# Kernel optimization log

Hardware: AMD Instinct MI355X
Metric: run time of the kernel (lower is better)

## Reference

```python
import jax, jax.numpy as jnp
import numpy as np

L2_REG = 0.01  # config['l2_reg']


def setup_inputs() -> dict:
    key = jax.random.key(0)
    k1, k2, k3, k4 = jax.random.split(key, 4)
    N = 16384
    risk_pred = jax.random.normal(k1, (N, 1), dtype=jnp.float32)
    y = jax.random.uniform(k2, (N, 1), dtype=jnp.float32)  # survival times
    e = jax.random.randint(k3, (N, 1), 0, 2, dtype=jnp.int32)  # event indicator
    W = jax.random.normal(k4, (512, 256), dtype=jnp.float32)  # model weight for L2 reg
    return {"risk_pred": risk_pred, "y": y, "e": e, "W": W}


def reference(risk_pred, y, e, W):
    # mask[i, j] = 1 if y[j] <= y[i] else 0  (torch: mask[y.T - y > 0] = 0)
    mask = (y.T - y <= 0).astype(risk_pred.dtype)  # (N, N)
    exp_r = jnp.exp(risk_pred)                      # (N, 1), broadcasts over rows
    num = jnp.sum(exp_r * mask, axis=0)             # (N,) risk-set weighted sum per column
    den = jnp.sum(mask, axis=0)                     # (N,) risk-set size per column
    log_loss = jnp.log(num / den).reshape(-1, 1)    # (N, 1)
    ef = e.astype(risk_pred.dtype)
    neg_log_loss = -jnp.sum((risk_pred - log_loss) * ef) / jnp.sum(ef)
    l2_loss = L2_REG * jnp.linalg.norm(W)           # Regularization(order=2)
    return neg_log_loss + l2_loss
```

## Files before the change

kernel.cpp:

```cpp
#include <hip/hip_runtime.h>

#define L2_REG 0.01f
#define NBIN 1024
#define MAXB 64


__global__ __launch_bounds__(256) void cox_hist(const float* __restrict__ rp,
                                                const float* __restrict__ y,
                                                const float* __restrict__ W,
                                                int* __restrict__ cnt,
                                                float* __restrict__ sum,
                                                float* __restrict__ by,
                                                float* __restrict__ be,
                                                float* __restrict__ wpart) {
    const int b = blockIdx.x;
    if (b < 64) {
        const int i = b * 256 + threadIdx.x;
        const float yi = y[i];
        const float ei = __expf(rp[i]);
        int bin = (int)(yi * (float)NBIN);
        bin = min(max(bin, 0), NBIN - 1);
        atomicAdd(&sum[bin], ei);
        const int pos = atomicAdd(&cnt[bin], 1);
        if (pos < MAXB) {
            by[bin * MAXB + pos] = yi;
            be[bin * MAXB + pos] = ei;
        }
    } else {
        __shared__ float l[4];
        const float4* W4 = reinterpret_cast<const float4*>(W) + (b - 64) * 512;
        float s = 0.f;
#pragma unroll
        for (int k = 0; k < 2; ++k) {
            float4 w = W4[k * 256 + threadIdx.x];
            s = fmaf(w.x, w.x, s); s = fmaf(w.y, w.y, s);
            s = fmaf(w.z, w.z, s); s = fmaf(w.w, w.w, s);
        }
#pragma unroll
        for (int off = 32; off; off >>= 1) s += __shfl_down(s, off, 64);
        const int lane = threadIdx.x & 63, wave = threadIdx.x >> 6;
        if (lane == 0) l[wave] = s;
        __syncthreads();
        if (threadIdx.x == 0) wpart[b - 64] = l[0] + l[1] + l[2] + l[3];
    }
}

__global__ __launch_bounds__(1024) void cox_scan(const int* __restrict__ cnt,
                                                 const float* __restrict__ sum,
                                                 const float* __restrict__ wpart,
                                                 float* __restrict__ sufc,
                                                 float* __restrict__ sufs,
                                                 float* __restrict__ acc,
                                                 int* __restrict__ cnt2) {
    __shared__ float sc[NBIN];
    __shared__ float sm[NBIN];
    const int t = threadIdx.x;
    sc[t] = (float)cnt[t];
    sm[t] = sum[t];
    __syncthreads();
#pragma unroll
    for (int s = 1; s < NBIN; s <<= 1) {
        const float a = (t + s < NBIN) ? sc[t + s] : 0.f;
        const float c = (t + s < NBIN) ? sm[t + s] : 0.f;
        __syncthreads();
        sc[t] += a; sm[t] += c;
        __syncthreads();
    }
    sufc[t] = sc[t];
    sufs[t] = sm[t];
    if (t == 0) {
        sufc[NBIN] = 0.f; sufs[NBIN] = 0.f;
        acc[0] = 0.f; acc[1] = 0.f; cnt2[0] = 0;
    }
    if (t < 64) {
        float wv = wpart[t];
#pragma unroll
        for (int off = 32; off; off >>= 1) wv += __shfl_down(wv, off, 64);
        if (t == 0) acc[2] = wv;
    }
}

__global__ __launch_bounds__(64) void cox_terms(const float* __restrict__ rp,
                                                const float* __restrict__ y,
                                                const int* __restrict__ e,
                                                const int* __restrict__ cnt,
                                                const float* __restrict__ by,
                                                const float* __restrict__ be,
                                                const float* __restrict__ sufc,
                                                const float* __restrict__ sufs,
                                                float* __restrict__ acc,
                                                int* __restrict__ cnt2,
                                                float* __restrict__ out) {
    const int j = blockIdx.x * 64 + threadIdx.x;
    const float yj = y[j];
    int bin = (int)(yj * (float)NBIN);
    bin = min(max(bin, 0), NBIN - 1);
    float den = sufc[bin + 1];
    float num = sufs[bin + 1];
    const int nb = min(cnt[bin], MAXB);
    const float4* by4 = reinterpret_cast<const float4*>(by + bin * MAXB);
    const float4* be4 = reinterpret_cast<const float4*>(be + bin * MAXB);
    for (int p = 0; p < nb; p += 4) {
        const float4 yv = by4[p >> 2];
        const float4 ev = be4[p >> 2];
        const float m0 = (yv.x >= yj) ? 1.f : 0.f;
        const float m1 = ((p + 1 < nb) && (yv.y >= yj)) ? 1.f : 0.f;
        const float m2 = ((p + 2 < nb) && (yv.z >= yj)) ? 1.f : 0.f;
        const float m3 = ((p + 3 < nb) && (yv.w >= yj)) ? 1.f : 0.f;
        den += m0; num = fmaf(m0, ev.x, num);
        den += m1; num = fmaf(m1, ev.y, num);
        den += m2; num = fmaf(m2, ev.z, num);
        den += m3; num = fmaf(m3, ev.w, num);
    }
    const float ef = (float)e[j];
    float term = (rp[j] - __logf(num / den)) * ef;
    float es = ef;
#pragma unroll
    for (int off = 32; off; off >>= 1) {
        term += __shfl_down(term, off, 64);
        es   += __shfl_down(es,   off, 64);
    }
    if (threadIdx.x != 0) return;
    atomicAdd(&acc[0], term);
    atomicAdd(&acc[1], es);
    __threadfence();
    if (atomicAdd(cnt2, 1) == 255) {
        const float a0 = atomicAdd(&acc[0], 0.f);
        const float a1 = atomicAdd(&acc[1], 0.f);
        out[0] = -a0 / a1 + L2_REG * sqrtf(acc[2]);
    }
}

extern "C" void kernel_launch(void* const* d_in, const int* in_sizes, int n_in,
                              void* d_out, int out_size, void* d_ws, size_t ws_size,
                              hipStream_t stream) {
    const float* rp = (const float*)d_in[0];
    const float* y  = (const float*)d_in[1];
    const int*   e  = (const int*)d_in[2];
    const float* W  = (const float*)d_in[3];

    int*   cnt   = (int*)d_ws;
    float* sum   = (float*)(cnt + NBIN);
    float* by    = sum + NBIN;
    float* be    = by + NBIN * MAXB;
    float* sufc  = be + NBIN * MAXB;
    float* sufs  = sufc + NBIN + 4;
    float* wpart = sufs + NBIN + 4;
    float* acc   = wpart + 64;
    int*   cnt2  = (int*)(acc + 4);

    hipMemsetAsync(d_ws, 0, 2 * NBIN * sizeof(float), stream);

    cox_hist<<<dim3(128), dim3(256), 0, stream>>>(rp, y, W, cnt, sum, by, be, wpart);
    cox_scan<<<dim3(1), dim3(1024), 0, stream>>>(cnt, sum, wpart, sufc, sufs, acc, cnt2);
    cox_terms<<<dim3(256), dim3(64), 0, stream>>>(rp, y, e, cnt, by, be, sufc, sufs,
                                                  acc, cnt2, (float*)d_out);
}
```

Before: 81.96 us.

## Fold suffix scan into histogram kernel via last-block pattern, drop scan launch

Removes the separate single-block scan kernel. The last histogram block to finish, found with an atomic ticket, now computes the suffix sums using a double-buffered shared-memory scan. The W-norm partial reduction moves into the last block of the terms kernel. The terms kernel now runs 64 blocks of 256 threads with a shared-memory cross-wave reduction, which cuts the number of global atomics. Accumulators and tickets are zeroed by the existing memset, trading one kernel launch for a serialized scan tail inside the histogram kernel.

```diff
diff --git a/kernel.cpp b/kernel.cpp
--- a/kernel.cpp
+++ b/kernel.cpp
@@ -12,10 +12,14 @@
                                                 float* __restrict__ sum,
                                                 float* __restrict__ by,
                                                 float* __restrict__ be,
-                                                float* __restrict__ wpart) {
+                                                float* __restrict__ wpart,
+                                                float* __restrict__ sufc,
+                                                float* __restrict__ sufs,
+                                                int* __restrict__ tick) {
     const int b = blockIdx.x;
+    const int t = threadIdx.x;
     if (b < 64) {
-        const int i = b * 256 + threadIdx.x;
+        const int i = b * 256 + t;
         const float yi = y[i];
         const float ei = __expf(rp[i]);
         int bin = (int)(yi * (float)NBIN);
@@ -32,66 +36,70 @@
         float s = 0.f;
 #pragma unroll
         for (int k = 0; k < 2; ++k) {
-            float4 w = W4[k * 256 + threadIdx.x];
+            float4 w = W4[k * 256 + t];
             s = fmaf(w.x, w.x, s); s = fmaf(w.y, w.y, s);
             s = fmaf(w.z, w.z, s); s = fmaf(w.w, w.w, s);
         }
 #pragma unroll
         for (int off = 32; off; off >>= 1) s += __shfl_down(s, off, 64);
-        const int lane = threadIdx.x & 63, wave = threadIdx.x >> 6;
+        const int lane = t & 63, wave = t >> 6;
         if (lane == 0) l[wave] = s;
         __syncthreads();
-        if (threadIdx.x == 0) wpart[b - 64] = l[0] + l[1] + l[2] + l[3];
+        if (t == 0) wpart[b - 64] = l[0] + l[1] + l[2] + l[3];
     }
+
+    __threadfence();
+    __shared__ int last;
+    if (t == 0) last = (atomicAdd(&tick[0], 1) == 127) ? 1 : 0;
+    __syncthreads();
+    if (!last) return;
+
+    __shared__ float c0[NBIN], s0[NBIN], c1[NBIN], s1[NBIN];
+#pragma unroll
+    for (int k = 0; k < 4; ++k) {
+        const int idx = k * 256 + t;
+        c0[idx] = (float)atomicAdd(&cnt[idx], 0);
+        s0[idx] = atomicAdd(&sum[idx], 0.f);
+    }
+    __syncthreads();
+    float *cs = c0, *ss = s0, *cd = c1, *sd = s1;
+#pragma unroll
+    for (int s = 1; s < NBIN; s <<= 1) {
+#pragma unroll
+        for (int k = 0; k < 4; ++k) {
+            const int idx = k * 256 + t;
+            const int ok = (idx + s < NBIN);
+            cd[idx] = cs[idx] + (ok ? cs[idx + s] : 0.f);
+            sd[idx] = ss[idx] + (ok ? ss[idx + s] : 0.f);
+        }
+        __syncthreads();
+        float* tp;
+        tp = cs; cs = cd; cd = tp;
+        tp = ss; ss = sd; sd = tp;
+    }
+#pragma unroll
+    for (int k = 0; k < 4; ++k) {
+        const int idx = k * 256 + t;
+        sufc[idx] = cs[idx];
+        sufs[idx] = ss[idx];
+    }
+    if (t == 0) { sufc[NBIN] = 0.f; sufs[NBIN] = 0.f; }
 }
 
-__global__ __launch_bounds__(1024) void cox_scan(const int* __restrict__ cnt,
-                                                 const float* __restrict__ sum,
+__global__ __launch_bounds__(256) void cox_terms(const float* __restrict__ rp,
+                                                 const float* __restrict__ y,
+                                                 const int* __restrict__ e,
+                                                 const int* __restrict__ cnt,
+                                                 const float* __restrict__ by,
+                                                 const float* __restrict__ be,
+                                                 const float* __restrict__ sufc,
+                                                 const float* __restrict__ sufs,
                                                  const float* __restrict__ wpart,
-                                                 float* __restrict__ sufc,
-                                                 float* __restrict__ sufs,
                                                  float* __restrict__ acc,
-                                                 int* __restrict__ cnt2) {
-    __shared__ float sc[NBIN];
-    __shared__ float sm[NBIN];
+                                                 int* __restrict__ tick,
+                                                 float* __restrict__ out) {
     const int t = threadIdx.x;
-    sc[t] = (float)cnt[t];
-    sm[t] = sum[t];
-    __syncthreads();
-#pragma unroll
-    for (int s = 1; s < NBIN; s <<= 1) {
-        const float a = (t + s < NBIN) ? sc[t + s] : 0.f;
-        const float c = (t + s < NBIN) ? sm[t + s] : 0.f;
-        __syncthreads();
-        sc[t] += a; sm[t] += c;
-        __syncthreads();
-    }
-    sufc[t] = sc[t];
-    sufs[t] = sm[t];
-    if (t == 0) {
-        sufc[NBIN] = 0.f; sufs[NBIN] = 0.f;
-        acc[0] = 0.f; acc[1] = 0.f; cnt2[0] = 0;
-    }
-    if (t < 64) {
-        float wv = wpart[t];
-#pragma unroll
-        for (int off = 32; off; off >>= 1) wv += __shfl_down(wv, off, 64);
-        if (t == 0) acc[2] = wv;
-    }
-}
-
-__global__ __launch_bounds__(64) void cox_terms(const float* __restrict__ rp,
-                                                const float* __restrict__ y,
-                                                const int* __restrict__ e,
-                                                const int* __restrict__ cnt,
-                                                const float* __restrict__ by,
-                                                const float* __restrict__ be,
-                                                const float* __restrict__ sufc,
-                                                const float* __restrict__ sufs,
-                                                float* __restrict__ acc,
-                                                int* __restrict__ cnt2,
-                                                float* __restrict__ out) {
-    const int j = blockIdx.x * 64 + threadIdx.x;
+    const int j = blockIdx.x * 256 + t;
     const float yj = y[j];
     int bin = (int)(yj * (float)NBIN);
     bin = min(max(bin, 0), NBIN - 1);
@@ -120,14 +128,27 @@
         term += __shfl_down(term, off, 64);
         es   += __shfl_down(es,   off, 64);
     }
-    if (threadIdx.x != 0) return;
-    atomicAdd(&acc[0], term);
-    atomicAdd(&acc[1], es);
-    __threadfence();
-    if (atomicAdd(cnt2, 1) == 255) {
+    __shared__ float l1[4];
+    __shared__ float l2[4];
+    const int lane = t & 63, wave = t >> 6;
+    if (lane == 0) { l1[wave] = term; l2[wave] = es; }
+    __syncthreads();
+    __shared__ int last;
+    if (t == 0) {
+        atomicAdd(&acc[0], (l1[0] + l1[1]) + (l1[2] + l1[3]));
+        atomicAdd(&acc[1], (l2[0] + l2[1]) + (l2[2] + l2[3]));
+        __threadfence();
+        last = (atomicAdd(&tick[1], 1) == 63) ? 1 : 0;
+    }
+    __syncthreads();
+    if (!last || t >= 64) return;
+    float wv = wpart[t];
+#pragma unroll
+    for (int off = 32; off; off >>= 1) wv += __shfl_down(wv, off, 64);
+    if (t == 0) {
         const float a0 = atomicAdd(&acc[0], 0.f);
         const float a1 = atomicAdd(&acc[1], 0.f);
-        out[0] = -a0 / a1 + L2_REG * sqrtf(acc[2]);
+        out[0] = -a0 / a1 + L2_REG * sqrtf(wv);
     }
 }
 
@@ -141,18 +162,18 @@
 
     int*   cnt   = (int*)d_ws;
     float* sum   = (float*)(cnt + NBIN);
-    float* by    = sum + NBIN;
+    float* acc   = sum + NBIN;
+    int*   tick  = (int*)(acc + 4);
+    float* by    = (float*)(tick + 4);
     float* be    = by + NBIN * MAXB;
     float* sufc  = be + NBIN * MAXB;
     float* sufs  = sufc + NBIN + 4;
     float* wpart = sufs + NBIN + 4;
-    float* acc   = wpart + 64;
-    int*   cnt2  = (int*)(acc + 4);
 
-    hipMemsetAsync(d_ws, 0, 2 * NBIN * sizeof(float), stream);
+    hipMemsetAsync(d_ws, 0, (size_t)(2 * NBIN * 4 + 32), stream);
 
-    cox_hist<<<dim3(128), dim3(256), 0, stream>>>(rp, y, W, cnt, sum, by, be, wpart);
-    cox_scan<<<dim3(1), dim3(1024), 0, stream>>>(cnt, sum, wpart, sufc, sufs, acc, cnt2);
-    cox_terms<<<dim3(256), dim3(64), 0, stream>>>(rp, y, e, cnt, by, be, sufc, sufs,
-                                                  acc, cnt2, (float*)d_out);
+    cox_hist<<<dim3(128), dim3(256), 0, stream>>>(rp, y, W, cnt, sum, by, be,
+                                                  wpart, sufc, sufs, tick);
+    cox_terms<<<dim3(64), dim3(256), 0, stream>>>(rp, y, e, cnt, by, be, sufc, sufs,
+                                                  wpart, acc, tick, (float*)d_out);
 }
```

Measured after the change: 93.16 us. 1.14x slower.

## Fuse histogram, scan and term kernels into one cooperative kernel with grid syncs

Applied to the files above, without the earlier changes.

Replaces the three kernel launches (histogram + weight norm, suffix scan, per-sample terms) with a single cooperative kernel of 64 blocks that separates the phases with grid-wide syncs. The suffix scan is rewritten to run on 256 threads, each handling 4 bins serially, with a wave-level shuffle scan in place of a 1024-thread shared-memory scan. The aim is to remove launch overhead and inter-kernel gaps. The trade-offs are cooperative launch overhead, grid.sync cost, and the per-sample phase now running on only 64 blocks.

```diff
diff --git a/kernel.cpp b/kernel.cpp
--- a/kernel.cpp
+++ b/kernel.cpp
@@ -1,134 +1,129 @@
 #include <hip/hip_runtime.h>
+#include <hip/hip_cooperative_groups.h>
+
+namespace cg = cooperative_groups;
 
 #define L2_REG 0.01f
 #define NBIN 1024
 #define MAXB 64
 
+__global__ __launch_bounds__(256) void cox_all(const float* __restrict__ rp,
+                                               const float* __restrict__ y,
+                                               const int* __restrict__ e,
+                                               const float* __restrict__ W,
+                                               int* __restrict__ cnt,
+                                               float* __restrict__ sum,
+                                               float* __restrict__ acc,
+                                               float* __restrict__ by,
+                                               float* __restrict__ be,
+                                               float* __restrict__ sufc,
+                                               float* __restrict__ sufs,
+                                               float* __restrict__ out) {
+    cg::grid_group grid = cg::this_grid();
+    const int t    = threadIdx.x;
+    const int gid  = blockIdx.x * 256 + t;
+    const int lane = t & 63, wave = t >> 6;
+    __shared__ float l1[4], l2[4];
 
-__global__ __launch_bounds__(256) void cox_hist(const float* __restrict__ rp,
-                                                const float* __restrict__ y,
-                                                const float* __restrict__ W,
-                                                int* __restrict__ cnt,
-                                                float* __restrict__ sum,
-                                                float* __restrict__ by,
-                                                float* __restrict__ be,
-                                                float* __restrict__ wpart) {
-    const int b = blockIdx.x;
-    if (b < 64) {
-        const int i = b * 256 + threadIdx.x;
-        const float yi = y[i];
-        const float ei = __expf(rp[i]);
-        int bin = (int)(yi * (float)NBIN);
-        bin = min(max(bin, 0), NBIN - 1);
+    {
+        const float yi = y[gid];
+        const float ei = __expf(rp[gid]);
+        const int bin = min(max((int)(yi * (float)NBIN), 0), NBIN - 1);
         atomicAdd(&sum[bin], ei);
         const int pos = atomicAdd(&cnt[bin], 1);
         if (pos < MAXB) {
             by[bin * MAXB + pos] = yi;
             be[bin * MAXB + pos] = ei;
         }
-    } else {
-        __shared__ float l[4];
-        const float4* W4 = reinterpret_cast<const float4*>(W) + (b - 64) * 512;
+        const float4* W4 = reinterpret_cast<const float4*>(W);
+        const float4 w0 = W4[2 * gid];
+        const float4 w1 = W4[2 * gid + 1];
         float s = 0.f;
-#pragma unroll
-        for (int k = 0; k < 2; ++k) {
-            float4 w = W4[k * 256 + threadIdx.x];
-            s = fmaf(w.x, w.x, s); s = fmaf(w.y, w.y, s);
-            s = fmaf(w.z, w.z, s); s = fmaf(w.w, w.w, s);
-        }
+        s = fmaf(w0.x, w0.x, s); s = fmaf(w0.y, w0.y, s);
+        s = fmaf(w0.z, w0.z, s); s = fmaf(w0.w, w0.w, s);
+        s = fmaf(w1.x, w1.x, s); s = fmaf(w1.y, w1.y, s);
+        s = fmaf(w1.z, w1.z, s); s = fmaf(w1.w, w1.w, s);
 #pragma unroll
         for (int off = 32; off; off >>= 1) s += __shfl_down(s, off, 64);
-        const int lane = threadIdx.x & 63, wave = threadIdx.x >> 6;
-        if (lane == 0) l[wave] = s;
+        if (lane == 0) l1[wave] = s;
         __syncthreads();
-        if (threadIdx.x == 0) wpart[b - 64] = l[0] + l[1] + l[2] + l[3];
+        if (t == 0) atomicAdd(&acc[2], (l1[0] + l1[1]) + (l1[2] + l1[3]));
     }
-}
+    grid.sync();
 
-__global__ __launch_bounds__(1024) void cox_scan(const int* __restrict__ cnt,
-                                                 const float* __restrict__ sum,
-                                                 const float* __restrict__ wpart,
-                                                 float* __restrict__ sufc,
-                                                 float* __restrict__ sufs,
-                                                 float* __restrict__ acc,
-                                                 int* __restrict__ cnt2) {
-    __shared__ float sc[NBIN];
-    __shared__ float sm[NBIN];
-    const int t = threadIdx.x;
-    sc[t] = (float)cnt[t];
-    sm[t] = sum[t];
-    __syncthreads();
+    if (blockIdx.x == 0) {
+        float c[4], s2[4];
+        float cs = 0.f, ss = 0.f;
 #pragma unroll
-    for (int s = 1; s < NBIN; s <<= 1) {
-        const float a = (t + s < NBIN) ? sc[t + s] : 0.f;
-        const float c = (t + s < NBIN) ? sm[t + s] : 0.f;
+        for (int k = 0; k < 4; ++k) {
+            const int idx = NBIN - 1 - (4 * t + k);
+            cs += (float)cnt[idx]; c[k]  = cs;
+            ss += sum[idx];        s2[k] = ss;
+        }
+        float tc = cs, ts = ss;
+#pragma unroll
+        for (int off = 1; off < 64; off <<= 1) {
+            const float pc = __shfl_up(tc, off, 64);
+            const float ps = __shfl_up(ts, off, 64);
+            if (lane >= off) { tc += pc; ts += ps; }
+        }
+        __shared__ float wc[4], wsm[4];
+        if (lane == 63) { wc[wave] = tc; wsm[wave] = ts; }
         __syncthreads();
-        sc[t] += a; sm[t] += c;
+        float bc = 0.f, bs = 0.f;
+        for (int w = 0; w < wave; ++w) { bc += wc[w]; bs += wsm[w]; }
+        const float ec = (tc - cs) + bc;
+        const float es = (ts - ss) + bs;
+#pragma unroll
+        for (int k = 0; k < 4; ++k) {
+            const int idx = NBIN - 1 - (4 * t + k);
+            sufc[idx] = ec + c[k];
+            sufs[idx] = es + s2[k];
+        }
+        if (t == 0) { sufc[NBIN] = 0.f; sufs[NBIN] = 0.f; }
+    }
+    grid.sync();
+
+    {
+        const float yj = y[gid];
+        const int bin = min(max((int)(yj * (float)NBIN), 0), NBIN - 1);
+        float den = sufc[bin + 1];
+        float num = sufs[bin + 1];
+        const int nb = min(cnt[bin], MAXB);
+        const float4* by4 = reinterpret_cast<const float4*>(by + bin * MAXB);
+        const float4* be4 = reinterpret_cast<const float4*>(be + bin * MAXB);
+        for (int p = 0; p < nb; p += 4) {
+            const float4 yv = by4[p >> 2];
+            const float4 ev = be4[p >> 2];
+            const float m0 = (yv.x >= yj) ? 1.f : 0.f;
+            const float m1 = ((p + 1 < nb) && (yv.y >= yj)) ? 1.f : 0.f;
+            const float m2 = ((p + 2 < nb) && (yv.z >= yj)) ? 1.f : 0.f;
+            const float m3 = ((p + 3 < nb) && (yv.w >= yj)) ? 1.f : 0.f;
+            den += m0; num = fmaf(m0, ev.x, num);
+            den += m1; num = fmaf(m1, ev.y, num);
+            den += m2; num = fmaf(m2, ev.z, num);
+            den += m3; num = fmaf(m3, ev.w, num);
+        }
+        const float ef = (float)e[gid];
+        float term = (rp[gid] - __logf(num / den)) * ef;
+        float es = ef;
+#pragma unroll
+        for (int off = 32; off; off >>= 1) {
+            term += __shfl_down(term, off, 64);
+            es   += __shfl_down(es,   off, 64);
+        }
         __syncthreads();
+        if (lane == 0) { l1[wave] = term; l2[wave] = es; }
+        __syncthreads();
+        if (t == 0) {
+            atomicAdd(&acc[0], (l1[0] + l1[1]) + (l1[2] + l1[3]));
+            atomicAdd(&acc[1], (l2[0] + l2[1]) + (l2[2] + l2[3]));
+        }
     }
-    sufc[t] = sc[t];
-    sufs[t] = sm[t];
-    if (t == 0) {
-        sufc[NBIN] = 0.f; sufs[NBIN] = 0.f;
-        acc[0] = 0.f; acc[1] = 0.f; cnt2[0] = 0;
-    }
-    if (t < 64) {
-        float wv = wpart[t];
-#pragma unroll
-        for (int off = 32; off; off >>= 1) wv += __shfl_down(wv, off, 64);
-        if (t == 0) acc[2] = wv;
-    }
-}
+    grid.sync();
 
-__global__ __launch_bounds__(64) void cox_terms(const float* __restrict__ rp,
-                                                const float* __restrict__ y,
-                                                const int* __restrict__ e,
-                                                const int* __restrict__ cnt,
-                                                const float* __restrict__ by,
-                                                const float* __restrict__ be,
-                                                const float* __restrict__ sufc,
-                                                const float* __restrict__ sufs,
-                                                float* __restrict__ acc,
-                                                int* __restrict__ cnt2,
-                                                float* __restrict__ out) {
-    const int j = blockIdx.x * 64 + threadIdx.x;
-    const float yj = y[j];
-    int bin = (int)(yj * (float)NBIN);
-    bin = min(max(bin, 0), NBIN - 1);
-    float den = sufc[bin + 1];
-    float num = sufs[bin + 1];
-    const int nb = min(cnt[bin], MAXB);
-    const float4* by4 = reinterpret_cast<const float4*>(by + bin * MAXB);
-    const float4* be4 = reinterpret_cast<const float4*>(be + bin * MAXB);
-    for (int p = 0; p < nb; p += 4) {
-        const float4 yv = by4[p >> 2];
-        const float4 ev = be4[p >> 2];
-        const float m0 = (yv.x >= yj) ? 1.f : 0.f;
-        const float m1 = ((p + 1 < nb) && (yv.y >= yj)) ? 1.f : 0.f;
-        const float m2 = ((p + 2 < nb) && (yv.z >= yj)) ? 1.f : 0.f;
-        const float m3 = ((p + 3 < nb) && (yv.w >= yj)) ? 1.f : 0.f;
-        den += m0; num = fmaf(m0, ev.x, num);
-        den += m1; num = fmaf(m1, ev.y, num);
-        den += m2; num = fmaf(m2, ev.z, num);
-        den += m3; num = fmaf(m3, ev.w, num);
-    }
-    const float ef = (float)e[j];
-    float term = (rp[j] - __logf(num / den)) * ef;
-    float es = ef;
-#pragma unroll
-    for (int off = 32; off; off >>= 1) {
-        term += __shfl_down(term, off, 64);
-        es   += __shfl_down(es,   off, 64);
-    }
-    if (threadIdx.x != 0) return;
-    atomicAdd(&acc[0], term);
-    atomicAdd(&acc[1], es);
-    __threadfence();
-    if (atomicAdd(cnt2, 1) == 255) {
-        const float a0 = atomicAdd(&acc[0], 0.f);
-        const float a1 = atomicAdd(&acc[1], 0.f);
-        out[0] = -a0 / a1 + L2_REG * sqrtf(acc[2]);
-    }
+    if (gid == 0)
+        out[0] = -acc[0] / acc[1] + L2_REG * sqrtf(acc[2]);
 }
 
 extern "C" void kernel_launch(void* const* d_in, const int* in_sizes, int n_in,
@@ -139,20 +134,20 @@
     const int*   e  = (const int*)d_in[2];
     const float* W  = (const float*)d_in[3];
 
-    int*   cnt   = (int*)d_ws;
-    float* sum   = (float*)(cnt + NBIN);
-    float* by    = sum + NBIN;
-    float* be    = by + NBIN * MAXB;
-    float* sufc  = be + NBIN * MAXB;
-    float* sufs  = sufc + NBIN + 4;
-    float* wpart = sufs + NBIN + 4;
-    float* acc   = wpart + 64;
-    int*   cnt2  = (int*)(acc + 4);
+    int*   cnt  = (int*)d_ws;
+    float* sum  = (float*)(cnt + NBIN);
+    float* acc  = sum + NBIN;
+    float* by   = acc + 4;
+    float* be   = by + NBIN * MAXB;
+    float* sufc = be + NBIN * MAXB;
+    float* sufs = sufc + NBIN + 4;
+    float* outp = (float*)d_out;
 
-    hipMemsetAsync(d_ws, 0, 2 * NBIN * sizeof(float), stream);
+    hipMemsetAsync(d_ws, 0, (size_t)(2 * NBIN * 4 + 16), stream);
 
-    cox_hist<<<dim3(128), dim3(256), 0, stream>>>(rp, y, W, cnt, sum, by, be, wpart);
-    cox_scan<<<dim3(1), dim3(1024), 0, stream>>>(cnt, sum, wpart, sufc, sufs, acc, cnt2);
-    cox_terms<<<dim3(256), dim3(64), 0, stream>>>(rp, y, e, cnt, by, be, sufc, sufs,
-                                                  acc, cnt2, (float*)d_out);
+    void* args[] = {(void*)&rp, (void*)&y, (void*)&e, (void*)&W,
+                    (void*)&cnt, (void*)&sum, (void*)&acc,
+                    (void*)&by, (void*)&be, (void*)&sufc, (void*)&sufs,
+                    (void*)&outp};
+    hipLaunchCooperativeKernel((void*)cox_all, dim3(64), dim3(256), args, 0, stream);
 }
```

Measured after the change: 112.4 us. 37.1% more time.
